# Kernel optimization log

Hardware: AMD Instinct MI355X
Metric: run time of the kernel (lower is better)

The kernel has to match this reference:

```python
import jax, jax.numpy as jnp
import numpy as np

B, SQ, SK = 2, 2048, 2048
D_MODEL, N_HEADS = 1024, 16
D_HEAD = D_MODEL // N_HEADS
LN_EPS = 1e-5


def _ln(x, w, b):
    # per-head LayerNorm over last dim (d_head)
    mu = jnp.mean(x, axis=-1, keepdims=True)
    var = jnp.mean(jnp.square(x - mu), axis=-1, keepdims=True)
    return (x - mu) * jax.lax.rsqrt(var + LN_EPS) * w + b


def setup_inputs() -> dict:
    key = jax.random.key(0)
    ks = jax.random.split(key, 8)
    sd = 1.0 / np.sqrt(D_MODEL)
    so = 1.0 / np.sqrt(D_HEAD)
    return {
        "x_q": jax.random.normal(ks[0], (B, SQ, D_MODEL), jnp.float32),
        "x_kv": jax.random.normal(ks[1], (B, SK, D_MODEL), jnp.float32),
        "mask": jnp.tril(jnp.ones((SQ, SK), dtype=bool)),  # causal
        "W_Q": jax.random.normal(ks[2], (N_HEADS, D_MODEL, D_HEAD), jnp.float32) * sd,
        "W_K": jax.random.normal(ks[3], (N_HEADS, D_MODEL, D_HEAD), jnp.float32) * sd,
        "W_V": jax.random.normal(ks[4], (N_HEADS, D_MODEL, D_HEAD), jnp.float32) * sd,
        "W_O": jax.random.normal(ks[5], (N_HEADS, D_HEAD, D_MODEL), jnp.float32) * so,
        "b_Q": jnp.zeros((N_HEADS, D_HEAD), jnp.float32),
        "b_K": jnp.zeros((N_HEADS, D_HEAD), jnp.float32),
        "b_V": jnp.zeros((N_HEADS, D_HEAD), jnp.float32),
        "b_O": jnp.zeros((D_MODEL,), jnp.float32),
        "ln1_w": jnp.ones((D_HEAD,), jnp.float32),
        "ln1_b": jnp.zeros((D_HEAD,), jnp.float32),
        "ln2_w": jnp.ones((D_HEAD,), jnp.float32),
        "ln2_b": jnp.zeros((D_HEAD,), jnp.float32),
    }


def reference(x_q, x_kv, mask, W_Q, W_K, W_V, W_O, b_Q, b_K, b_V, b_O,
              ln1_w, ln1_b, ln2_w, ln2_b):
    # QKV projections: b s d, n d h -> b s n h
    q = jnp.einsum('bsd,ndh->bsnh', x_q, W_Q) + b_Q
    k = jnp.einsum('bsd,ndh->bsnh', x_kv, W_K) + b_K
    v = jnp.einsum('bsd,ndh->bsnh', x_kv, W_V) + b_V
    # QK-norm (ln_first=False, rope=None -> just apply LN after projections)
    q = _ln(q, ln1_w, ln1_b)
    k = _ln(k, ln2_w, ln2_b)
    # NOTE: no 1/sqrt(d_head) scaling, matching the original module
    att = jnp.einsum('bqnh,bknh->bnqk', q, k)
    att = jnp.where(mask, att, -jnp.inf)
    probas = jax.nn.softmax(att, axis=-1)
    z = jnp.einsum('bnqk,bknh->bqnh', probas, v)
    out = jnp.einsum('bqnh,nhd->bqd', z, W_O) + b_O
    return (out, k, v)
```

## Files before the change

kernel.cpp:

```cpp
#include <hip/hip_runtime.h>
#include <hip/hip_bf16.h>

#define B_   2
#define SQ_  2048
#define DM_  1024
#define NH_  16
#define DH_  64

typedef __attribute__((ext_vector_type(8))) short          bf16x8;
typedef __attribute__((ext_vector_type(8))) unsigned short u16x8;
typedef __attribute__((ext_vector_type(4))) float          f32x4;

__device__ __forceinline__ unsigned short f2bf(float f) {
    union { __hip_bfloat16 h; unsigned short u; } c;
    c.h = __float2bfloat16(f);
    return c.u;
}
__device__ __forceinline__ float gsum16(float v) {
    v += __shfl_xor(v, 1);
    v += __shfl_xor(v, 2);
    v += __shfl_xor(v, 4);
    v += __shfl_xor(v, 8);
    return v;
}

__device__ __forceinline__ void gll16(const unsigned short* g, unsigned short* l) {
    __builtin_amdgcn_global_load_lds(
        (const __attribute__((address_space(1))) unsigned int*)g,
        (__attribute__((address_space(3))) unsigned int*)l,
        16, 0, 0);
}

__global__ __launch_bounds__(256) void prep_all(
    const float* __restrict__ W_Q, const float* __restrict__ W_K,
    const float* __restrict__ W_V, const float* __restrict__ W_O,
    const float* __restrict__ x_q, const float* __restrict__ x_kv,
    unsigned short* __restrict__ WTq, unsigned short* __restrict__ WTkv,
    unsigned short* __restrict__ WTo,
    unsigned short* __restrict__ xqbf, unsigned short* __restrict__ xkvbf)
{
    const int bid = blockIdx.x, tid = threadIdx.x;
    if (bid >= 1024) {
        const int cid = bid - 1024;
        const float* src = (cid < 256) ? x_q : x_kv;
        unsigned short* dst = (cid < 256) ? xqbf : xkvbf;
        const size_t base = (size_t)(cid & 255) * 16384 + tid * 4;
#pragma unroll
        for (int i = 0; i < 16; ++i) {
            const float4 v = *(const float4*)(src + base + i * 1024);
            ushort4 o;
            o.x = f2bf(v.x); o.y = f2bf(v.y); o.z = f2bf(v.z); o.w = f2bf(v.w);
            *(ushort4*)(dst + base + i * 1024) = o;
        }
        return;
    }
    __shared__ float t[64][65];
    const float* src; unsigned short* dst; int R, C, r0, c0;
    if (bid < 768) {
        const int which = bid >> 8, rem = bid & 255;
        const int rblk = rem & 15, zz = rem >> 4;
        src = (which == 0) ? W_Q : (which == 1) ? W_K : W_V;
        dst = (which == 0) ? WTq : (which == 1) ? WTkv : (WTkv + (1u << 20));
        src += (size_t)65536 * zz;
        dst += (size_t)65536 * zz;
        R = 1024; C = 64; r0 = rblk * 64; c0 = 0;
    } else {
        const int rem = bid - 768;
        src = W_O; dst = WTo; R = 1024; C = 1024;
        r0 = (rem & 15) * 64; c0 = (rem >> 4) * 64;
    }
    const int lr = tid >> 6, lc = tid & 63;
#pragma unroll
    for (int i = 0; i < 16; ++i)
        t[lr + i * 4][lc] = src[(size_t)(r0 + lr + i * 4) * C + c0 + lc];
    __syncthreads();
    const int u = tid & 15, w0 = tid >> 4;
#pragma unroll
    for (int i = 0; i < 4; ++i) {
        const int cl = w0 + i * 16;
        ushort4 o;
        o.x = f2bf(t[4 * u + 0][cl]);
        o.y = f2bf(t[4 * u + 1][cl]);
        o.z = f2bf(t[4 * u + 2][cl]);
        o.w = f2bf(t[4 * u + 3][cl]);
        *(ushort4*)&dst[(size_t)(c0 + cl) * R + r0 + 4 * u] = o;
    }
}

template <int TM, int MODE>
__device__ __forceinline__ void gemm_body(
    unsigned short (*__restrict__ As)[64], unsigned short (*__restrict__ Bs)[64],
    int bx, int by, const unsigned short* __restrict__ Abf,
    const unsigned short* __restrict__ WT,
    const float* __restrict__ biasK, const float* __restrict__ biasV,
    const float* __restrict__ lnw, const float* __restrict__ lnb,
    float* __restrict__ Cf, float* __restrict__ Cf2,
    unsigned short* __restrict__ Cb, unsigned short* __restrict__ CbT, int tid)
{
    constexpr int MI = TM / 32;
    constexpr int AJ = TM / 32;

    const int m0 = by * TM;
    const int c0 = bx * 128;

    const int wid = tid >> 6, lane = tid & 63;
    const int wm = (wid >> 1) * (TM / 2);
    const int wn = (wid & 1) * 64;
    const int l15 = lane & 15, qd = lane >> 4;

    const int srow  = tid >> 3;
    const int pslot = tid & 7;
    const int sslot = pslot ^ (srow & 7);
    const unsigned short* Ag = Abf + (size_t)(m0 + srow) * 1024 + sslot * 8;
    const unsigned short* Bg = WT  + (size_t)(c0 + srow) * 1024 + sslot * 8;
    unsigned short* Al = &As[srow][pslot * 8];
    unsigned short* Bl = &Bs[srow][pslot * 8];

    const f32x4 zero4 = {0.f, 0.f, 0.f, 0.f};
    f32x4 acc[MI][4];
#pragma unroll
    for (int mi = 0; mi < MI; ++mi)
#pragma unroll
        for (int ni = 0; ni < 4; ++ni) acc[mi][ni] = zero4;

    const int r7 = l15 & 7;

    for (int kb = 0; kb < 16; ++kb) {
        const size_t kof = (size_t)kb * 64;
        __syncthreads();
#pragma unroll
        for (int j = 0; j < AJ; ++j)
            gll16(Ag + (size_t)j * 32 * 1024 + kof, Al + j * 32 * 64);
#pragma unroll
        for (int j = 0; j < 4; ++j)
            gll16(Bg + (size_t)j * 32 * 1024 + kof, Bl + j * 32 * 64);
        __syncthreads();
#pragma unroll
        for (int ks = 0; ks < 2; ++ks) {
            const int cs = ((ks * 4 + qd) ^ r7) * 8;
            bf16x8 af[MI], bfr[4];
#pragma unroll
            for (int mi = 0; mi < MI; ++mi)
                af[mi] = *(const bf16x8*)&As[wm + mi * 16 + l15][cs];
#pragma unroll
            for (int ni = 0; ni < 4; ++ni)
                bfr[ni] = *(const bf16x8*)&Bs[wn + ni * 16 + l15][cs];
#pragma unroll
            for (int mi = 0; mi < MI; ++mi)
#pragma unroll
                for (int ni = 0; ni < 4; ++ni)
                    acc[mi][ni] = __builtin_amdgcn_mfma_f32_16x16x32_bf16(
                        af[mi], bfr[ni], acc[mi][ni], 0, 0, 0);
        }
    }

    const float* bias = (MODE == 1 && c0 >= 1024) ? biasV : biasK;
    float bv[4];
#pragma unroll
    for (int ni = 0; ni < 4; ++ni) bv[ni] = bias[(c0 + wn + ni * 16 + l15) & 1023];
#pragma unroll
    for (int mi = 0; mi < MI; ++mi)
#pragma unroll
        for (int ni = 0; ni < 4; ++ni)
#pragma unroll
            for (int r = 0; r < 4; ++r) acc[mi][ni][r] += bv[ni];

    if constexpr (MODE != 2) {
        const bool doLN = (MODE == 0) || (c0 < 1024);
        if (doLN) {
            float w4[4], lb4[4];
#pragma unroll
            for (int ni = 0; ni < 4; ++ni) {
                w4[ni]  = lnw[ni * 16 + l15];
                lb4[ni] = lnb[ni * 16 + l15];
            }
#pragma unroll
            for (int mi = 0; mi < MI; ++mi)
#pragma unroll
                for (int r = 0; r < 4; ++r) {
                    float s1 = acc[mi][0][r] + acc[mi][1][r] + acc[mi][2][r] + acc[mi][3][r];
                    const float mu = gsum16(s1) * (1.0f / 64.0f);
                    float s2 = acc[mi][0][r] * acc[mi][0][r] + acc[mi][1][r] * acc[mi][1][r]
                             + acc[mi][2][r] * acc[mi][2][r] + acc[mi][3][r] * acc[mi][3][r];
                    const float var = gsum16(s2) * (1.0f / 64.0f) - mu * mu;
                    const float rstd = rsqrtf(var + 1e-5f);
#pragma unroll
                    for (int ni = 0; ni < 4; ++ni)
                        acc[mi][ni][r] = (acc[mi][ni][r] - mu) * rstd * w4[ni] + lb4[ni];
                }
        }
    }

    if constexpr (MODE == 0) {
#pragma unroll
        for (int mi = 0; mi < MI; ++mi)
#pragma unroll
            for (int r = 0; r < 4; ++r) {
                const size_t grow = m0 + wm + mi * 16 + qd * 4 + r;
#pragma unroll
                for (int ni = 0; ni < 4; ++ni)
                    Cb[grow * 1024 + c0 + wn + ni * 16 + l15] = f2bf(acc[mi][ni][r]);
            }
    } else if constexpr (MODE == 2) {
#pragma unroll
        for (int mi = 0; mi < MI; ++mi)
#pragma unroll
            for (int r = 0; r < 4; ++r) {
                const size_t grow = m0 + wm + mi * 16 + qd * 4 + r;
#pragma unroll
                for (int ni = 0; ni < 4; ++ni)
                    Cf[grow * 1024 + c0 + wn + ni * 16 + l15] = acc[mi][ni][r];
            }
    } else {
        if (c0 < 1024) {
#pragma unroll
            for (int mi = 0; mi < MI; ++mi)
#pragma unroll
                for (int r = 0; r < 4; ++r) {
                    const size_t grow = m0 + wm + mi * 16 + qd * 4 + r;
#pragma unroll
                    for (int ni = 0; ni < 4; ++ni) {
                        const int gcol = c0 + wn + ni * 16 + l15;
                        Cf[grow * 1024 + gcol] = acc[mi][ni][r];
                        Cb[grow * 1024 + gcol] = f2bf(acc[mi][ni][r]);
                    }
                }
        } else {
#pragma unroll
            for (int mi = 0; mi < MI; ++mi) {
                const int growb = m0 + wm + mi * 16 + qd * 4;
                const int bb_ = growb >> 11, ss = growb & 2047;
#pragma unroll
                for (int ni = 0; ni < 4; ++ni) {
                    const int gv = c0 - 1024 + wn + ni * 16 + l15;
                    const int hh = gv >> 6, dd = gv & 63;
#pragma unroll
                    for (int r = 0; r < 4; ++r)
                        Cf2[(size_t)(growb + r) * 1024 + gv] = acc[mi][ni][r];
                    ushort4 w;
                    w.x = f2bf(acc[mi][ni][0]); w.y = f2bf(acc[mi][ni][1]);
                    w.z = f2bf(acc[mi][ni][2]); w.w = f2bf(acc[mi][ni][3]);
                    *(ushort4*)&CbT[(((size_t)bb_ * NH_ + hh) * DH_ + dd) * SQ_ + ss] = w;
                }
            }
        }
    }
}

__global__ __launch_bounds__(256) void qkv_fused(
    const unsigned short* __restrict__ xqbf, const unsigned short* __restrict__ xkvbf,
    const unsigned short* __restrict__ WTq, const unsigned short* __restrict__ WTkv,
    const float* __restrict__ b_Q, const float* __restrict__ b_K,
    const float* __restrict__ b_V,
    const float* __restrict__ ln1w, const float* __restrict__ ln1b,
    const float* __restrict__ ln2w, const float* __restrict__ ln2b,
    float* __restrict__ kout, float* __restrict__ vout,
    unsigned short* __restrict__ qz, unsigned short* __restrict__ kbf,
    unsigned short* __restrict__ vbfT)
{
    __shared__ __align__(16) unsigned short As[64][64];
    __shared__ __align__(16) unsigned short Bs[128][64];
    const int bid = blockIdx.x, tid = threadIdx.x;
    if (bid < 1024) {
        gemm_body<64, 1>(As, Bs, bid & 15, bid >> 4, xkvbf, WTkv, b_K, b_V,
                         ln2w, ln2b, kout, vout, kbf, vbfT, tid);
    } else {
        const int b2 = bid - 1024;
        gemm_body<64, 0>(As, Bs, b2 & 7, b2 >> 3, xqbf, WTq, b_Q, nullptr,
                         ln1w, ln1b, nullptr, nullptr, qz, nullptr, tid);
    }
}

__global__ __launch_bounds__(256) void o_gemm(
    const unsigned short* __restrict__ zbf, const unsigned short* __restrict__ WTo,
    const float* __restrict__ b_O, float* __restrict__ out)
{
    __shared__ __align__(16) unsigned short As[64][64];
    __shared__ __align__(16) unsigned short Bs[128][64];
    gemm_body<64, 2>(As, Bs, blockIdx.x, blockIdx.y, zbf, WTo, b_O, nullptr,
                     nullptr, nullptr, out, nullptr, nullptr, nullptr, threadIdx.x);
}

__global__ __launch_bounds__(256) void attn_mfma(
    unsigned short* __restrict__ qz, const unsigned short* __restrict__ kbf,
    const unsigned short* __restrict__ vbfT)
{
    __shared__ __align__(16) unsigned short Ks[2][64][72];
    __shared__ __align__(16) unsigned short VsT[2][64][72];
    __shared__ __align__(16) unsigned short Ps[64][72];

    const int tid = threadIdx.x;
    const int h = blockIdx.y, b = blockIdx.z;
    const int wid = tid >> 6, lane = tid & 63;
    const int l15 = lane & 15, qd = lane >> 4;
    const int srow = tid >> 2, scol = (tid & 3) * 16;

    const size_t kbase = (size_t)b * SQ_ * DM_ + (size_t)h * DH_;
    const size_t vbase = ((size_t)b * NH_ + h) * DH_ * (size_t)SQ_;
    const f32x4 zero4 = {0.f, 0.f, 0.f, 0.f};
    const float LOG2E = 1.44269504f, MBIAS = 46.1662413f;

    for (int pass = 0; pass < 2; ++pass) {
        const int qt = pass ? blockIdx.x : 31 - blockIdx.x;

        bf16x8 qf[2];
        {
            const unsigned short* qp =
                qz + kbase + (size_t)(qt * 64 + wid * 16 + l15) * DM_ + qd * 8;
            qf[0] = *(const bf16x8*)(qp);
            qf[1] = *(const bf16x8*)(qp + 32);
        }

        f32x4 z[4];
#pragma unroll
        for (int ni = 0; ni < 4; ++ni) z[ni] = zero4;
        float l_i = 0.f;

        {
            const unsigned short* ks = kbf + kbase + (size_t)srow * DM_ + scol;
            const u16x8 a0 = *(const u16x8*)(ks);
            const u16x8 a1 = *(const u16x8*)(ks + 8);
            const unsigned short* vs = vbfT + vbase + (size_t)srow * SQ_ + scol;
            const u16x8 b0 = *(const u16x8*)(vs);
            const u16x8 b1 = *(const u16x8*)(vs + 8);
            *(u16x8*)&Ks[0][srow][scol + 0]  = a0;
            *(u16x8*)&Ks[0][srow][scol + 8]  = a1;
            *(u16x8*)&VsT[0][srow][scol + 0] = b0;
            *(u16x8*)&VsT[0][srow][scol + 8] = b1;
        }
        __syncthreads();

        for (int kt = 0; kt <= qt; ++kt) {
            const int cur = kt & 1;

            u16x8 kr0, kr1, vr0, vr1;
            if (kt < qt) {
                const unsigned short* ks =
                    kbf + kbase + (size_t)((kt + 1) * 64 + srow) * DM_ + scol;
                kr0 = *(const u16x8*)(ks);
                kr1 = *(const u16x8*)(ks + 8);
                const unsigned short* vs =
                    vbfT + vbase + (size_t)srow * SQ_ + (kt + 1) * 64 + scol;
                vr0 = *(const u16x8*)(vs);
                vr1 = *(const u16x8*)(vs + 8);
            }

            f32x4 s[4];
#pragma unroll
            for (int mi = 0; mi < 4; ++mi) s[mi] = zero4;
#pragma unroll
            for (int ks2 = 0; ks2 < 2; ++ks2)
#pragma unroll
                for (int mi = 0; mi < 4; ++mi) {
                    const bf16x8 af =
                        *(const bf16x8*)&Ks[cur][mi * 16 + l15][ks2 * 32 + qd * 8];
                    s[mi] = __builtin_amdgcn_mfma_f32_16x16x32_bf16(af, qf[ks2], s[mi], 0, 0, 0);
                }

            if (kt == qt) {
#pragma unroll
                for (int mi = 0; mi < 4; ++mi)
#pragma unroll
                    for (int r = 0; r < 4; ++r)
                        if (mi * 16 + qd * 4 + r > wid * 16 + l15) s[mi][r] = -3.0e38f;
            }

            float ts[4];
#pragma unroll
            for (int mi = 0; mi < 4; ++mi) {
#pragma unroll
                for (int r = 0; r < 4; ++r)
                    s[mi][r] = __builtin_amdgcn_exp2f(fmaf(s[mi][r], LOG2E, -MBIAS));
                ts[mi] = (s[mi][0] + s[mi][1]) + (s[mi][2] + s[mi][3]);
            }
            float rs = (ts[0] + ts[1]) + (ts[2] + ts[3]);
            rs += __shfl_xor(rs, 16);
            rs += __shfl_xor(rs, 32);
            l_i += rs;

#pragma unroll
            for (int mi = 0; mi < 4; ++mi) {
                ushort4 w;
                w.x = f2bf(s[mi][0]); w.y = f2bf(s[mi][1]);
                w.z = f2bf(s[mi][2]); w.w = f2bf(s[mi][3]);
                *(ushort4*)&Ps[wid * 16 + l15][mi * 16 + qd * 4] = w;
            }

#pragma unroll
            for (int ks2 = 0; ks2 < 2; ++ks2) {
                const bf16x8 ap = *(const bf16x8*)&Ps[wid * 16 + l15][ks2 * 32 + qd * 8];
#pragma unroll
                for (int ni = 0; ni < 4; ++ni) {
                    const bf16x8 bv =
                        *(const bf16x8*)&VsT[cur][ni * 16 + l15][ks2 * 32 + qd * 8];
                    z[ni] = __builtin_amdgcn_mfma_f32_16x16x32_bf16(ap, bv, z[ni], 0, 0, 0);
                }
            }

            if (kt < qt) {
                *(u16x8*)&Ks[cur ^ 1][srow][scol + 0]  = kr0;
                *(u16x8*)&Ks[cur ^ 1][srow][scol + 8]  = kr1;
                *(u16x8*)&VsT[cur ^ 1][srow][scol + 0] = vr0;
                *(u16x8*)&VsT[cur ^ 1][srow][scol + 8] = vr1;
            }
            __syncthreads();
        }

        const float linv = 1.0f / l_i;
#pragma unroll
        for (int r = 0; r < 4; ++r) {
            const float lr_ = __shfl(linv, qd * 4 + r);
            const size_t row = (size_t)qt * 64 + wid * 16 + qd * 4 + r;
#pragma unroll
            for (int ni = 0; ni < 4; ++ni)
                qz[kbase + row * DM_ + ni * 16 + l15] = f2bf(z[ni][r] * lr_);
        }
    }
}

extern "C" void kernel_launch(void* const* d_in, const int* in_sizes, int n_in,
                              void* d_out, int out_size, void* d_ws, size_t ws_size,
                              hipStream_t stream)
{
    const float* x_q  = (const float*)d_in[0];
    const float* x_kv = (const float*)d_in[1];
    const float* W_Q  = (const float*)d_in[3];
    const float* W_K  = (const float*)d_in[4];
    const float* W_V  = (const float*)d_in[5];
    const float* W_O  = (const float*)d_in[6];
    const float* b_Q  = (const float*)d_in[7];
    const float* b_K  = (const float*)d_in[8];
    const float* b_V  = (const float*)d_in[9];
    const float* b_O  = (const float*)d_in[10];
    const float* ln1w = (const float*)d_in[11];
    const float* ln1b = (const float*)d_in[12];
    const float* ln2w = (const float*)d_in[13];
    const float* ln2b = (const float*)d_in[14];

    const size_t NTOK = (size_t)B_ * SQ_;
    float* out  = (float*)d_out;
    float* kout = out + NTOK * DM_;
    float* vout = kout + NTOK * DM_;

    unsigned short* xqbf  = (unsigned short*)out;
    unsigned short* xkvbf = xqbf + (1u << 22);

    unsigned short* wsu  = (unsigned short*)d_ws;
    unsigned short* WTq  = wsu;
    unsigned short* WTkv = WTq + (1u << 20);
    unsigned short* WTo  = WTkv + (2u << 20);
    unsigned short* qz   = WTo + (1u << 20);
    unsigned short* kbf  = qz + (1u << 22);
    unsigned short* vbfT = kbf + (1u << 22);

    prep_all<<<1536, 256, 0, stream>>>(W_Q, W_K, W_V, W_O, x_q, x_kv,
                                       WTq, WTkv, WTo, xqbf, xkvbf);

    qkv_fused<<<1536, 256, 0, stream>>>(xqbf, xkvbf, WTq, WTkv, b_Q, b_K, b_V,
                                        ln1w, ln1b, ln2w, ln2b,
                                        kout, vout, qz, kbf, vbfT);

    attn_mfma<<<dim3(16, NH_, B_), 256, 0, stream>>>(qz, kbf, vbfT);

    o_gemm<<<dim3(8, 64), 256, 0, stream>>>(qz, WTo, b_O, out);
}
```

Baseline: 231.7 us.

## Load K fragments directly into registers in attention; split prep conversion blocks

The attention kernel no longer stages K tiles through shared memory. Each wave loads its own MFMA K fragments straight from global memory into registers and prefetches the next tile right after the QK MFMAs. This removes the LDS writes and reads for K and shrinks LDS use, at the cost of more registers and uncoalesced per-lane 16-byte global loads that each of the four waves repeats. Separately, the x conversion in prep_all is split across twice as many blocks, each doing half the work, to spread the memory-bound cast more widely.

```diff
diff --git a/kernel.cpp b/kernel.cpp
--- a/kernel.cpp
+++ b/kernel.cpp
@@ -42,11 +42,11 @@
     const int bid = blockIdx.x, tid = threadIdx.x;
     if (bid >= 1024) {
         const int cid = bid - 1024;
-        const float* src = (cid < 256) ? x_q : x_kv;
-        unsigned short* dst = (cid < 256) ? xqbf : xkvbf;
-        const size_t base = (size_t)(cid & 255) * 16384 + tid * 4;
-#pragma unroll
-        for (int i = 0; i < 16; ++i) {
+        const float* src = (cid < 512) ? x_q : x_kv;
+        unsigned short* dst = (cid < 512) ? xqbf : xkvbf;
+        const size_t base = (size_t)(cid & 511) * 8192 + tid * 4;
+#pragma unroll
+        for (int i = 0; i < 8; ++i) {
             const float4 v = *(const float4*)(src + base + i * 1024);
             ushort4 o;
             o.x = f2bf(v.x); o.y = f2bf(v.y); o.z = f2bf(v.z); o.w = f2bf(v.w);
@@ -285,7 +285,6 @@
     unsigned short* __restrict__ qz, const unsigned short* __restrict__ kbf,
     const unsigned short* __restrict__ vbfT)
 {
-    __shared__ __align__(16) unsigned short Ks[2][64][72];
     __shared__ __align__(16) unsigned short VsT[2][64][72];
     __shared__ __align__(16) unsigned short Ps[64][72];
 
@@ -299,6 +298,19 @@
     const size_t vbase = ((size_t)b * NH_ + h) * DH_ * (size_t)SQ_;
     const f32x4 zero4 = {0.f, 0.f, 0.f, 0.f};
     const float LOG2E = 1.44269504f, MBIAS = 46.1662413f;
+
+    const unsigned short* kfb = kbf + kbase + (size_t)l15 * DM_ + qd * 8;
+
+#define LOADK(kt_)                                                             \
+    {                                                                          \
+        const unsigned short* kp = kfb + (size_t)(kt_) * 64 * DM_;             \
+        _Pragma("unroll")                                                      \
+        for (int ks2 = 0; ks2 < 2; ++ks2)                                      \
+            _Pragma("unroll")                                                  \
+            for (int mi = 0; mi < 4; ++mi)                                     \
+                kf[ks2][mi] = *(const bf16x8*)(kp + (size_t)mi * 16 * DM_ +    \
+                                               ks2 * 32);                      \
+    }
 
     for (int pass = 0; pass < 2; ++pass) {
         const int qt = pass ? blockIdx.x : 31 - blockIdx.x;
@@ -311,20 +323,18 @@
             qf[1] = *(const bf16x8*)(qp + 32);
         }
 
+        bf16x8 kf[2][4];
+        LOADK(0)
+
         f32x4 z[4];
 #pragma unroll
         for (int ni = 0; ni < 4; ++ni) z[ni] = zero4;
         float l_i = 0.f;
 
         {
-            const unsigned short* ks = kbf + kbase + (size_t)srow * DM_ + scol;
-            const u16x8 a0 = *(const u16x8*)(ks);
-            const u16x8 a1 = *(const u16x8*)(ks + 8);
             const unsigned short* vs = vbfT + vbase + (size_t)srow * SQ_ + scol;
             const u16x8 b0 = *(const u16x8*)(vs);
             const u16x8 b1 = *(const u16x8*)(vs + 8);
-            *(u16x8*)&Ks[0][srow][scol + 0]  = a0;
-            *(u16x8*)&Ks[0][srow][scol + 8]  = a1;
             *(u16x8*)&VsT[0][srow][scol + 0] = b0;
             *(u16x8*)&VsT[0][srow][scol + 8] = b1;
         }
@@ -333,12 +343,8 @@
         for (int kt = 0; kt <= qt; ++kt) {
             const int cur = kt & 1;
 
-            u16x8 kr0, kr1, vr0, vr1;
+            u16x8 vr0, vr1;
             if (kt < qt) {
-                const unsigned short* ks =
-                    kbf + kbase + (size_t)((kt + 1) * 64 + srow) * DM_ + scol;
-                kr0 = *(const u16x8*)(ks);
-                kr1 = *(const u16x8*)(ks + 8);
                 const unsigned short* vs =
                     vbfT + vbase + (size_t)srow * SQ_ + (kt + 1) * 64 + scol;
                 vr0 = *(const u16x8*)(vs);
@@ -351,11 +357,11 @@
 #pragma unroll
             for (int ks2 = 0; ks2 < 2; ++ks2)
 #pragma unroll
-                for (int mi = 0; mi < 4; ++mi) {
-                    const bf16x8 af =
-                        *(const bf16x8*)&Ks[cur][mi * 16 + l15][ks2 * 32 + qd * 8];
-                    s[mi] = __builtin_amdgcn_mfma_f32_16x16x32_bf16(af, qf[ks2], s[mi], 0, 0, 0);
-                }
+                for (int mi = 0; mi < 4; ++mi)
+                    s[mi] = __builtin_amdgcn_mfma_f32_16x16x32_bf16(
+                        kf[ks2][mi], qf[ks2], s[mi], 0, 0, 0);
+
+            if (kt < qt) LOADK(kt + 1)
 
             if (kt == qt) {
 #pragma unroll
@@ -398,8 +404,6 @@
             }
 
             if (kt < qt) {
-                *(u16x8*)&Ks[cur ^ 1][srow][scol + 0]  = kr0;
-                *(u16x8*)&Ks[cur ^ 1][srow][scol + 8]  = kr1;
                 *(u16x8*)&VsT[cur ^ 1][srow][scol + 0] = vr0;
                 *(u16x8*)&VsT[cur ^ 1][srow][scol + 8] = vr1;
             }
@@ -416,6 +420,7 @@
                 qz[kbase + row * DM_ + ni * 16 + l15] = f2bf(z[ni][r] * lr_);
         }
     }
+#undef LOADK
 }
 
 extern "C" void kernel_launch(void* const* d_in, const int* in_sizes, int n_in,
@@ -453,7 +458,7 @@
     unsigned short* kbf  = qz + (1u << 22);
     unsigned short* vbfT = kbf + (1u << 22);
 
-    prep_all<<<1536, 256, 0, stream>>>(W_Q, W_K, W_V, W_O, x_q, x_kv,
+    prep_all<<<2048, 256, 0, stream>>>(W_Q, W_K, W_V, W_O, x_q, x_kv,
                                        WTq, WTkv, WTo, xqbf, xkvbf);
 
     qkv_fused<<<1536, 256, 0, stream>>>(xqbf, xkvbf, WTq, WTkv, b_Q, b_K, b_V,
```

New measurement: 261.2 us. 1.13x slower.
